# Kernel tuning notes

Measured on AMD Instinct MI355X. Metric: run time of the kernel, lower is better.

The kernel has to match this reference:

```python
import jax, jax.numpy as jnp
import numpy as np

B, T, D, H, QK, V, M = 2, 2048, 1024, 16, 64, 64, 1024
SOFTCAP = 50.0


def apply_rope(x, positions, max_wavelength=10000.0):
    # x: (B, T, H, d), positions: (T,)
    d = x.shape[-1]
    fraction = 2.0 * jnp.arange(d // 2, dtype=jnp.float32) / d
    timescale = max_wavelength ** fraction                      # (d/2,)
    sinusoid = positions.astype(jnp.float32)[:, None] / timescale  # (T, d/2)
    sin = jnp.sin(sinusoid)[:, None, :]  # (T, 1, d/2) broadcasts over heads
    cos = jnp.cos(sinusoid)[:, None, :]
    x1, x2 = jnp.split(x, 2, axis=-1)
    out = jnp.concatenate([x1 * cos - x2 * sin, x2 * cos + x1 * sin], axis=-1)
    return out.astype(x.dtype)


def rms_norm(x, scale, eps=1e-6):
    var = jnp.mean(jnp.square(x.astype(jnp.float32)), axis=-1, keepdims=True)
    normed = x * jax.lax.rsqrt(var + eps).astype(x.dtype)
    return normed * (1.0 + scale).astype(x.dtype)


def setup_inputs() -> dict:
    key = jax.random.key(0)
    ks = jax.random.split(key, 10)
    s = 0.02
    # key-padding mask: per-batch kv valid lengths (all rows have >=1536 valid keys)
    kv_lens = jnp.array([1536, 2048], dtype=jnp.int32)
    mask = (jnp.arange(T)[None, :] < kv_lens[:, None])  # (B, Tk)
    mask = jnp.broadcast_to(mask[:, None, None, :], (B, 1, T, T))
    return {
        "q": jax.random.normal(ks[0], (B, T, D), jnp.float32),
        "kv": jax.random.normal(ks[1], (B, T, D), jnp.float32),
        "mask": mask,
        "q_positions": jnp.arange(T, dtype=jnp.int32),
        "kv_positions": jnp.arange(T, dtype=jnp.int32),
        "wq": jax.random.normal(ks[2], (D, H * QK), jnp.float32) * s,
        "bq": jnp.zeros((H * QK,), jnp.float32),
        "wk": jax.random.normal(ks[3], (D, H * QK), jnp.float32) * s,
        "bk": jnp.zeros((H * QK,), jnp.float32),
        "wv": jax.random.normal(ks[4], (D, H * V), jnp.float32) * s,
        "bv": jnp.zeros((H * V,), jnp.float32),
        "q_scale": jnp.zeros((QK,), jnp.float32),
        "k_scale": jnp.zeros((QK,), jnp.float32),
        "wo": jax.random.normal(ks[5], (H * V, M), jnp.float32) * s,
        "bo": jnp.zeros((M,), jnp.float32),
    }


def reference(q, kv, mask, q_positions, kv_positions,
              wq, bq, wk, bk, wv, bv, q_scale, k_scale, wo, bo):
    qh = (q @ wq + bq).reshape(B, T, H, QK)
    kh = (kv @ wk + bk).reshape(B, T, H, QK)
    vh = (kv @ wv + bv).reshape(B, T, H, V)
    # QK RMSNorm
    qh = rms_norm(qh, q_scale)
    kh = rms_norm(kh, k_scale)
    # RoPE
    qh = apply_rope(qh, q_positions)
    kh = apply_rope(kh, kv_positions)
    # softcapped, masked attention
    logits = jnp.einsum("bthd,bThd->bhtT", qh, kh) / np.sqrt(QK).astype(jnp.float32)
    logits = SOFTCAP * jnp.tanh(logits / SOFTCAP)
    logits = jnp.where(mask, logits, -1e9)
    log_probs = jax.nn.log_softmax(logits, axis=-1)
    probs = jnp.exp(log_probs)
    probs = jnp.where(mask, probs, 0.0)
    # normalized attention entropy (B, H, T)
    entropy = -jnp.sum(probs * log_probs, axis=-1) / jnp.log(mask.sum(axis=-1))
    attn = jnp.einsum("bhtT,bThd->bthd", probs, vh).reshape(B, T, H * V)
    out = attn @ wo + bo
    return out, entropy
```

## Files before the change

### kernel.cpp

```cpp
#include <hip/hip_runtime.h>

#define BB 2
#define TT 2048
#define DD 1024
#define HH 16
#define QKD 64
#define VD 64
#define MD 1024

typedef _Float16 half4 __attribute__((ext_vector_type(4)));
typedef _Float16 half8 __attribute__((ext_vector_type(8)));
typedef __fp16 fp16x2 __attribute__((ext_vector_type(2)));
typedef float f32x4 __attribute__((ext_vector_type(4)));
typedef unsigned short us8 __attribute__((ext_vector_type(8)));
typedef unsigned short us4 __attribute__((ext_vector_type(4)));

__device__ __forceinline__ unsigned short f2h(float x){
    union { _Float16 h; unsigned short u; } c; c.h = (_Float16)x; return c.u;
}

__device__ __forceinline__ void gl16(const void* g, void* l){
    __builtin_amdgcn_global_load_lds(
        (const __attribute__((address_space(1))) void*)g,
        (__attribute__((address_space(3))) void*)l, 16, 0, 0);
}

__global__ __launch_bounds__(256) void k_prep(const float* __restrict__ q,
                                              const float* __restrict__ kv,
                                              unsigned short* __restrict__ q_bf,
                                              unsigned short* __restrict__ kv_bf,
                                              const float* __restrict__ w0,
                                              const float* __restrict__ w1,
                                              const float* __restrict__ w2,
                                              const float* __restrict__ w3,
                                              unsigned short* __restrict__ o0,
                                              unsigned short* __restrict__ o1,
                                              unsigned short* __restrict__ o2,
                                              unsigned short* __restrict__ o3,
                                              const int* __restrict__ qpos,
                                              const int* __restrict__ kpos,
                                              float* __restrict__ tabq,
                                              float* __restrict__ tabk,
                                              const unsigned char* __restrict__ mask,
                                              int* __restrict__ kvlen){
    __shared__ float smem[64*65];
    int bid = blockIdx.x, tid = threadIdx.x;
    if (bid < 8192){
        const int n = BB*TT*DD/4;
        int idx = bid*256 + tid;
        const float* src = (idx < n) ? q : kv;
        unsigned short* dst = (idx < n) ? q_bf : kv_bf;
        int i = ((idx < n) ? idx : idx - n)*4;
        const float4 v = *(const float4*)(src + i);
        us4 o; o.x = f2h(v.x); o.y = f2h(v.y); o.z = f2h(v.z); o.w = f2h(v.w);
        *(us4*)(dst + i) = o;
    } else if (bid < 9216){
        int idx2 = bid - 8192;
        int z = idx2 >> 8;
        int rc2 = idx2 & 255;
        const float* in = (z==0) ? w0 : (z==1) ? w1 : (z==2) ? w2 : w3;
        unsigned short* out = (z==0) ? o0 : (z==1) ? o1 : (z==2) ? o2 : o3;
        float (*ts)[65] = (float(*)[65])smem;
        int r0 = (rc2 & 15)*64, c0 = (rc2 >> 4)*64;
        int lr = tid >> 4, lc = (tid & 15)*4;
#pragma unroll
        for (int i = 0; i < 4; ++i){
            const float4 v = *(const float4*)(in + (long)(r0 + lr + i*16)*1024 + c0 + lc);
            ts[lr+i*16][lc+0] = v.x; ts[lr+i*16][lc+1] = v.y;
            ts[lr+i*16][lc+2] = v.z; ts[lr+i*16][lc+3] = v.w;
        }
        __syncthreads();
        int oc = tid >> 2, rc = (tid & 3)*16;
        int ocp = oc;
        if (z < 2){
            int blk = oc >> 4;
            ocp = (blk == 1) ? oc + 16 : ((blk == 2) ? oc - 16 : oc);
        }
        us8 o0v, o1v;
#pragma unroll
        for (int j = 0; j < 8; ++j){ o0v[j] = f2h(ts[rc+j][ocp]); o1v[j] = f2h(ts[rc+8+j][ocp]); }
        *(us8*)(out + (long)(c0+oc)*1024 + r0 + rc)     = o0v;
        *(us8*)(out + (long)(c0+oc)*1024 + r0 + rc + 8) = o1v;
    } else if (bid < 9728){
        int gi = (bid - 9216)*256 + tid;
        const int* pos = (gi < 65536) ? qpos : kpos;
        float* tab = (gi < 65536) ? tabq : tabk;
        int idx = gi & 65535;
        int t = idx >> 5, f = idx & 31;
        float invts = expf(-((float)f*(1.f/32.f)) * 9.210340371976184f);
        float ph = (float)pos[t]*invts;
        ((float2*)tab)[idx] = make_float2(sinf(ph), cosf(ph));
    } else {
        int* red = (int*)smem;
        int b = bid - 9728;
        bool bytemode = (mask[1] != 0);
        int cnt = 0;
        for (int j = tid; j < TT; j += 256){
            long e = (long)b*TT*TT + j;
            if (bytemode) cnt += (mask[e] != 0);
            else          cnt += (((const unsigned int*)mask)[e] != 0);
        }
        red[tid] = cnt; __syncthreads();
        for (int s = 128; s > 0; s >>= 1){ if (tid < s) red[tid] += red[tid+s]; __syncthreads(); }
        if (tid == 0) kvlen[b] = red[0];
    }
}

#define GEMM_CORE(A_, Bt_, abase, bbase)                                            \
    int srow = l >> 3;                                                              \
    int scol = ((l & 7) ^ srow)*8;                                                  \
    int swb = lg ^ (li & 7);                                                        \
    const unsigned short* ga[4]; const unsigned short* gb[2];                       \
    _Pragma("unroll")                                                               \
    for (int i = 0; i < 4; ++i) ga[i] = A_  + (long)(m0 + w*32 + i*8 + srow)*1024 + scol; \
    _Pragma("unroll")                                                               \
    for (int i = 0; i < 2; ++i) gb[i] = Bt_ + (long)(n0 + w*16 + i*8 + srow)*1024 + scol; \
    _Pragma("unroll")                                                               \
    for (int i = 0; i < 4; ++i) gl16(ga[i], abase + (w*32 + i*8)*128);              \
    _Pragma("unroll")                                                               \
    for (int i = 0; i < 2; ++i) gl16(gb[i], bbase + (w*16 + i*8)*128);              \
    __syncthreads();                                                                \
    for (int ks = 0; ks < 16; ++ks){                                                \
        int cur = ks & 1;                                                           \
        if (ks + 1 < 16){                                                           \
            char* an = abase + (cur^1)*16384;                                       \
            char* bn = bbase + (cur^1)*8192;                                        \
            _Pragma("unroll")                                                       \
            for (int i = 0; i < 4; ++i){ ga[i] += 64; gl16(ga[i], an + (w*32 + i*8)*128); } \
            _Pragma("unroll")                                                       \
            for (int i = 0; i < 2; ++i){ gb[i] += 64; gl16(gb[i], bn + (w*16 + i*8)*128); } \
        }                                                                           \
        const char* ac = abase + cur*16384;                                         \
        const char* bc = bbase + cur*8192;                                          \
        _Pragma("unroll")                                                           \
        for (int kk = 0; kk < 2; ++kk){                                             \
            int co = ((kk*4) ^ swb)*16;                                             \
            half8 af[4], bf[2];                                                     \
            _Pragma("unroll")                                                       \
            for (int mi = 0; mi < 4; ++mi) af[mi] = *(const half8*)(ac + (wm + mi*16 + li)*128 + co); \
            _Pragma("unroll")                                                       \
            for (int ni = 0; ni < 2; ++ni) bf[ni] = *(const half8*)(bc + (wn + ni*16 + li)*128 + co); \
            _Pragma("unroll")                                                       \
            for (int mi = 0; mi < 4; ++mi)                                          \
                _Pragma("unroll")                                                   \
                for (int ni = 0; ni < 2; ++ni)                                      \
                    acc[mi][ni] = __builtin_amdgcn_mfma_f32_16x16x32_f16(af[mi], bf[ni], acc[mi][ni], 0, 0, 0); \
        }                                                                           \
        __syncthreads();                                                            \
    }

__global__ __launch_bounds__(256) void k_gemm3(const unsigned short* __restrict__ q_bf,
                                               const unsigned short* __restrict__ kv_bf,
                                               const unsigned short* __restrict__ wqt,
                                               const unsigned short* __restrict__ wkt,
                                               const unsigned short* __restrict__ wvt,
                                               const float* __restrict__ bq,
                                               const float* __restrict__ bk,
                                               const float* __restrict__ bv,
                                               const float* __restrict__ qscale,
                                               const float* __restrict__ kscale,
                                               const float* __restrict__ tabq,
                                               const float* __restrict__ tabk,
                                               unsigned short* __restrict__ Qr,
                                               unsigned short* __restrict__ Kr,
                                               unsigned short* __restrict__ VTb){
    __shared__ float4 smem_[3072];
    char* abase = (char*)smem_;
    char* bbase = abase + 32768;
    int flat = blockIdx.x;
    int virt = (flat & 7)*192 + (flat >> 3);
    int z = virt >> 9;
    int rem = virt & 511;
    int m0 = (rem >> 4)*128;
    int nx = rem & 15;
    int n0 = nx*64;
    const unsigned short* A  = (z == 0) ? q_bf : kv_bf;
    const unsigned short* Bt = (z == 0) ? wqt : (z == 1) ? wkt : wvt;

    int tid = threadIdx.x, l = tid & 63, w = tid >> 6;
    int lg = l >> 4, li = l & 15;
    int wm = (w >> 1)*64, wn = (w & 1)*32;
    f32x4 zero = {0.f,0.f,0.f,0.f};
    f32x4 acc[4][2];
#pragma unroll
    for (int mi = 0; mi < 4; ++mi){ acc[mi][0] = zero; acc[mi][1] = zero; }
    GEMM_CORE(A, Bt, abase, bbase)

    int hd = nx;
    if (z < 2){
        const float* bias  = (z == 0) ? bq : bk;
        const float* scale = (z == 0) ? qscale : kscale;
        const float* tab   = (z == 0) ? tabq : tabk;
        unsigned short* out = (z == 0) ? Qr : Kr;
        float* hs = (float*)smem_;
        int d0 = (wn >> 1) + li;
        float b0 = bias[hd*64 + d0];
        float b1 = bias[hd*64 + d0 + 32];
        float ssp[4][4];
#pragma unroll
        for (int mi = 0; mi < 4; ++mi)
#pragma unroll
            for (int r = 0; r < 4; ++r){
                float x0 = acc[mi][0][r] + b0;
                float x1 = acc[mi][1][r] + b1;
                ssp[mi][r] = x0*x0 + x1*x1;
            }
#pragma unroll
        for (int m = 1; m < 16; m <<= 1)
#pragma unroll
            for (int mi = 0; mi < 4; ++mi)
#pragma unroll
                for (int r = 0; r < 4; ++r) ssp[mi][r] += __shfl_xor(ssp[mi][r], m);
        if (li == 0){
#pragma unroll
            for (int mi = 0; mi < 4; ++mi)
#pragma unroll
                for (int r = 0; r < 4; ++r)
                    hs[(wm + mi*16 + lg*4 + r)*2 + (w & 1)] = ssp[mi][r];
        }
        __syncthreads();
        float sc0 = 1.f + scale[d0];
        float sc1 = 1.f + scale[d0 + 32];
#pragma unroll
        for (int mi = 0; mi < 4; ++mi)
#pragma unroll
            for (int r = 0; r < 4; ++r){
                int row = wm + mi*16 + lg*4 + r;
                float ss = hs[row*2] + hs[row*2 + 1];
                float rstd = rsqrtf(ss*(1.f/64.f) + 1e-6f);
                float x0 = (acc[mi][0][r] + b0)*rstd*sc0;
                float x1 = (acc[mi][1][r] + b1)*rstd*sc1;
                int gm = m0 + row;
                int bb = gm >> 11, t = gm & 2047;
                float2 scv = ((const float2*)tab)[t*32 + d0];
                float o0 = x0*scv.y - x1*scv.x;
                float o1 = x1*scv.y + x0*scv.x;
                long obase = ((long)(bb*HH + hd)*TT + t)*64;
                out[obase + d0]      = f2h(o0);
                out[obase + d0 + 32] = f2h(o1);
            }
    } else {
        float* Tt = (float*)smem_;
#pragma unroll
        for (int mi = 0; mi < 4; ++mi)
#pragma unroll
            for (int ni = 0; ni < 2; ++ni){
                int col = wn + ni*16 + li;
                float bb = bv[hd*64 + col];
#pragma unroll
                for (int r = 0; r < 4; ++r)
                    Tt[col*133 + wm + mi*16 + lg*4 + r] = acc[mi][ni][r] + bb;
            }
        __syncthreads();
        int bb2 = m0 >> 11, t0 = m0 & 2047;
        int vd = tid >> 2, sg = (tid & 3)*32;
        long ob = ((long)(bb2*HH + hd)*64 + vd)*TT + t0 + sg;
#pragma unroll
        for (int c = 0; c < 4; ++c){
            us8 o;
#pragma unroll
            for (int j = 0; j < 8; ++j) o[j] = f2h(Tt[vd*133 + sg + c*8 + j]);
            *(us8*)(VTb + ob + c*8) = o;
        }
    }
}

__global__ __launch_bounds__(256) void k_gemm(const unsigned short* __restrict__ A,
                                              const unsigned short* __restrict__ Bt,
                                              const float* __restrict__ bias,
                                              float* __restrict__ C, int N){
    __shared__ float4 smem_[3072];
    char* abase = (char*)smem_;
    char* bbase = abase + 32768;
    int flat = blockIdx.x;
    int virt = (flat & 7)*64 + (flat >> 3);
    int m0 = (virt >> 4)*128, n0 = (virt & 15)*64;
    int tid = threadIdx.x, l = tid & 63, w = tid >> 6;
    int lg = l >> 4, li = l & 15;
    int wm = (w >> 1)*64, wn = (w & 1)*32;
    f32x4 zero = {0.f,0.f,0.f,0.f};
    f32x4 acc[4][2];
#pragma unroll
    for (int mi = 0; mi < 4; ++mi){ acc[mi][0] = zero; acc[mi][1] = zero; }
    GEMM_CORE(A, Bt, abase, bbase)
#pragma unroll
    for (int mi = 0; mi < 4; ++mi){
#pragma unroll
        for (int ni = 0; ni < 2; ++ni){
            int row = m0 + wm + mi*16 + lg*4;
            int col = n0 + wn + ni*16 + li;
            float bb = bias[col];
#pragma unroll
            for (int r = 0; r < 4; ++r)
                C[(long)(row + r)*N + col] = acc[mi][ni][r] + bb;
        }
    }
}

__global__ __launch_bounds__(256) void k_attn(const unsigned short* __restrict__ Qr,
                                              const unsigned short* __restrict__ Kr,
                                              const unsigned short* __restrict__ VT,
                                              const int* __restrict__ kvlen,
                                              unsigned short* __restrict__ attnb,
                                              float* __restrict__ ent){
    __shared__ unsigned short Ks[2][64][64];
    __shared__ unsigned short Vs[2][64][64];
    int tid = threadIdx.x;
    int l = tid & 63, w = tid >> 6;
    int lg = l >> 4, li = l & 15;
    int flat = blockIdx.x;
    int xcd = flat & 7;
    int idx = flat >> 3;
    int qt = idx & 31;
    int g = idx >> 5;
    int bh = xcd*2 + (g & 1) + (g >> 1)*16;
    int b = bh >> 4, h = bh & 15;
    long qk0 = (long)bh * TT * 64;
    long vt0 = (long)bh * 64 * TT;
    int kvl = kvlen[b];
    int q0 = qt*64 + w*16;

    half8 qf[2];
#pragma unroll
    for (int kk = 0; kk < 2; ++kk)
        qf[kk] = *(const half8*)(Qr + qk0 + (long)(q0 + li)*64 + kk*32 + lg*8);

    int srow = l >> 3;
    int scol = ((l & 7) ^ srow)*8;
    const unsigned short* gK0 = Kr + qk0 + (long)(w*8 + srow)*64 + scol;
    const unsigned short* gK1 = gK0 + 32*64;
    const unsigned short* gV0 = VT + vt0 + (long)(w*8 + srow)*TT + scol;
    const unsigned short* gV1 = gV0 + (long)32*TT;
    char* ksb = (char*)Ks;
    char* vsb = (char*)Vs;
    int swb = (lg >> 1) ^ (li & 7);
    int off8 = (lg & 1)*8;

    gl16(gK0, ksb + w*8*128);
    gl16(gK1, ksb + (32 + w*8)*128);
    gl16(gV0, vsb + w*8*128);
    gl16(gV1, vsb + (32 + w*8)*128);
    __syncthreads();

    f32x4 zero = {0.f,0.f,0.f,0.f};
    f32x4 oacc[4];
#pragma unroll
    for (int jv = 0; jv < 4; ++jv) oacc[jv] = zero;
    float l4[4]  = {0.f,0.f,0.f,0.f};
    float s14[4] = {0.f,0.f,0.f,0.f};

    const float PA = 0.18033688f;
    const float PB = -3.7570183e-7f;

    int nkv = (kvl + 63) >> 6;
    for (int kt = 0; kt < nkv; ++kt){
        int cur = kt & 1;
        const char* kc = ksb + cur*8192;
        const char* vc = vsb + cur*8192;
        if (kt + 1 < nkv){
            gK0 += 4096; gK1 += 4096;
            gV0 += 64;   gV1 += 64;
            char* kn = ksb + (cur^1)*8192;
            char* vn = vsb + (cur^1)*8192;
            gl16(gK0, kn + w*8*128);
            gl16(gK1, kn + (32 + w*8)*128);
            gl16(gV0, vn + w*8*128);
            gl16(gV1, vn + (32 + w*8)*128);
        }
        f32x4 sacc[4];
#pragma unroll
        for (int jt = 0; jt < 4; ++jt) sacc[jt] = zero;
#pragma unroll
        for (int kk = 0; kk < 2; ++kk){
            int co = ((kk*4 + lg) ^ (li & 7))*16;
#pragma unroll
            for (int jt = 0; jt < 4; ++jt){
                half8 kf = *(const half8*)(kc + (jt*16 + li)*128 + co);
                sacc[jt] = __builtin_amdgcn_mfma_f32_16x16x32_f16(kf, qf[kk], sacc[jt], 0, 0, 0);
            }
        }
        float xs2[4][4];
        bool tail = (kt*64 + 64 > kvl);
        if (tail){
#pragma unroll
            for (int jt = 0; jt < 4; ++jt){
#pragma unroll
                for (int r = 0; r < 4; ++r){
                    float u = sacc[jt][r];
                    float v = u*(PA + u*u*PB);
                    xs2[jt][r] = (kt*64 + jt*16 + lg*4 + r < kvl) ? v : -1e30f;
                }
            }
        } else {
#pragma unroll
            for (int jt = 0; jt < 4; ++jt){
#pragma unroll
                for (int r = 0; r < 4; ++r){
                    float u = sacc[jt][r];
                    xs2[jt][r] = u*(PA + u*u*PB);
                }
            }
        }
        float p[4][4];
#pragma unroll
        for (int jt = 0; jt < 4; ++jt){
#pragma unroll
            for (int r = 0; r < 4; ++r){
                float pp = exp2f(xs2[jt][r]);
                p[jt][r] = pp;
                l4[r]  += pp;
                s14[r] += pp * xs2[jt][r];
            }
        }
        half4 pa[4];
#pragma unroll
        for (int kk = 0; kk < 4; ++kk){
            union { half4 v; fp16x2 h2[2]; } up;
            up.h2[0] = __builtin_amdgcn_cvt_pkrtz(p[kk][0], p[kk][1]);
            up.h2[1] = __builtin_amdgcn_cvt_pkrtz(p[kk][2], p[kk][3]);
            pa[kk] = up.v;
        }
#pragma unroll
        for (int kk = 0; kk < 4; ++kk){
            int co = (((kk*2) ^ swb))*16 + off8;
#pragma unroll
            for (int jv = 0; jv < 4; ++jv){
                half4 vf = *(const half4*)(vc + (jv*16 + li)*128 + co);
                oacc[jv] = __builtin_amdgcn_mfma_f32_16x16x16f16(pa[kk], vf, oacc[jv], 0, 0, 0);
            }
        }
        __syncthreads();
    }

    float l_r  = (l4[0] + l4[1]) + (l4[2] + l4[3]);
    float s1_r = (s14[0] + s14[1]) + (s14[2] + s14[3]);
    l_r  += __shfl_xor(l_r, 16);  l_r  += __shfl_xor(l_r, 32);
    s1_r += __shfl_xor(s1_r, 16); s1_r += __shfl_xor(s1_r, 32);

    float invl = 1.f / l_r;
    float invr[4];
#pragma unroll
    for (int r = 0; r < 4; ++r) invr[r] = __shfl(invl, lg*4 + r);
#pragma unroll
    for (int jv = 0; jv < 4; ++jv){
#pragma unroll
        for (int r = 0; r < 4; ++r){
            int qrow = q0 + lg*4 + r;
            attnb[((long)b*TT + qrow)*1024 + h*64 + jv*16 + li] = f2h(oacc[jv][r]*invr[r]);
        }
    }
    if (l < 16){
        const float LN2 = 0.6931471805599453f;
        float lse = logf(l_r);
        float s1n = s1_r*LN2;
        ent[(long)bh*TT + q0 + li] = (lse - s1n*invl) / logf((float)kvl);
    }
}

extern "C" void kernel_launch(void* const* d_in, const int* in_sizes, int n_in,
                              void* d_out, int out_size, void* d_ws, size_t ws_size,
                              hipStream_t stream){
    (void)in_sizes; (void)n_in; (void)out_size; (void)ws_size;
    const float* q      = (const float*)d_in[0];
    const float* kv     = (const float*)d_in[1];
    const unsigned char* mask = (const unsigned char*)d_in[2];
    const int*   qpos   = (const int*)d_in[3];
    const int*   kpos   = (const int*)d_in[4];
    const float* wq     = (const float*)d_in[5];
    const float* bq     = (const float*)d_in[6];
    const float* wk     = (const float*)d_in[7];
    const float* bk     = (const float*)d_in[8];
    const float* wv     = (const float*)d_in[9];
    const float* bv     = (const float*)d_in[10];
    const float* qscale = (const float*)d_in[11];
    const float* kscale = (const float*)d_in[12];
    const float* wo     = (const float*)d_in[13];
    const float* bo     = (const float*)d_in[14];
    float* out = (float*)d_out;
    float* ent = out + (long)BB*TT*MD;

    char* ws = (char*)d_ws;
    unsigned short* wqt   = (unsigned short*)(ws);
    unsigned short* wkt   = (unsigned short*)(ws + 2097152L);
    unsigned short* wvt   = (unsigned short*)(ws + 4194304L);
    unsigned short* wot   = (unsigned short*)(ws + 6291456L);
    unsigned short* q_bf  = (unsigned short*)(ws + 8388608L);
    unsigned short* kv_bf = (unsigned short*)(ws + 16777216L);
    unsigned short* Qr    = (unsigned short*)(ws + 25165824L);
    unsigned short* Kr    = (unsigned short*)(ws + 33554432L);
    unsigned short* VTb   = (unsigned short*)(ws + 41943040L);
    unsigned short* attnb = (unsigned short*)(ws + 50331648L);
    float*          tabq  = (float*)(ws + 58720256L);
    float*          tabk  = (float*)(ws + 59244544L);
    int*            kvln  = (int*)(ws + 59768832L);

    k_prep<<<9730, 256, 0, stream>>>(q, kv, q_bf, kv_bf,
                                     wq, wk, wv, wo, wqt, wkt, wvt, wot,
                                     qpos, kpos, tabq, tabk, mask, kvln);

    k_gemm3<<<1536, 256, 0, stream>>>(q_bf, kv_bf, wqt, wkt, wvt,
                                      bq, bk, bv, qscale, kscale,
                                      tabq, tabk, Qr, Kr, VTb);

    k_attn<<<1024, 256, 0, stream>>>(Qr, Kr, VTb, kvln, attnb, ent);

    k_gemm<<<512, 256, 0, stream>>>(attnb, wot, bo, out, 1024);
}
```

Before: 143.8 us.

## Load K and V fragments directly from global memory in attention kernel

Removes the double-buffered LDS staging of K and V tiles (global_load_lds plus barriers) and has each wave read its MFMA fragments straight from global memory through the cache. This drops the per-iteration __syncthreads and the shared-memory footprint, which may raise occupancy. In exchange, each of the four waves in a block redundantly fetches the same K/V tiles, and the loads are exposed in the loop without explicit prefetch, relying on L1/L2 hits and the compiler to hide latency.

```diff
diff --git a/kernel.cpp b/kernel.cpp
--- a/kernel.cpp
+++ b/kernel.cpp
@@ -303,8 +303,6 @@
                                               const int* __restrict__ kvlen,
                                               unsigned short* __restrict__ attnb,
                                               float* __restrict__ ent){
-    __shared__ unsigned short Ks[2][64][64];
-    __shared__ unsigned short Vs[2][64][64];
     int tid = threadIdx.x;
     int l = tid & 63, w = tid >> 6;
     int lg = l >> 4, li = l & 15;
@@ -325,23 +323,6 @@
     for (int kk = 0; kk < 2; ++kk)
         qf[kk] = *(const half8*)(Qr + qk0 + (long)(q0 + li)*64 + kk*32 + lg*8);
 
-    int srow = l >> 3;
-    int scol = ((l & 7) ^ srow)*8;
-    const unsigned short* gK0 = Kr + qk0 + (long)(w*8 + srow)*64 + scol;
-    const unsigned short* gK1 = gK0 + 32*64;
-    const unsigned short* gV0 = VT + vt0 + (long)(w*8 + srow)*TT + scol;
-    const unsigned short* gV1 = gV0 + (long)32*TT;
-    char* ksb = (char*)Ks;
-    char* vsb = (char*)Vs;
-    int swb = (lg >> 1) ^ (li & 7);
-    int off8 = (lg & 1)*8;
-
-    gl16(gK0, ksb + w*8*128);
-    gl16(gK1, ksb + (32 + w*8)*128);
-    gl16(gV0, vsb + w*8*128);
-    gl16(gV1, vsb + (32 + w*8)*128);
-    __syncthreads();
-
     f32x4 zero = {0.f,0.f,0.f,0.f};
     f32x4 oacc[4];
 #pragma unroll
@@ -352,30 +333,19 @@
     const float PA = 0.18033688f;
     const float PB = -3.7570183e-7f;
 
+    const unsigned short* Kp = Kr + qk0 + (long)li*64 + lg*8;
+    const unsigned short* Vp = VT + vt0 + (long)li*TT + lg*4;
+
     int nkv = (kvl + 63) >> 6;
     for (int kt = 0; kt < nkv; ++kt){
-        int cur = kt & 1;
-        const char* kc = ksb + cur*8192;
-        const char* vc = vsb + cur*8192;
-        if (kt + 1 < nkv){
-            gK0 += 4096; gK1 += 4096;
-            gV0 += 64;   gV1 += 64;
-            char* kn = ksb + (cur^1)*8192;
-            char* vn = vsb + (cur^1)*8192;
-            gl16(gK0, kn + w*8*128);
-            gl16(gK1, kn + (32 + w*8)*128);
-            gl16(gV0, vn + w*8*128);
-            gl16(gV1, vn + (32 + w*8)*128);
-        }
         f32x4 sacc[4];
 #pragma unroll
         for (int jt = 0; jt < 4; ++jt) sacc[jt] = zero;
 #pragma unroll
         for (int kk = 0; kk < 2; ++kk){
-            int co = ((kk*4 + lg) ^ (li & 7))*16;
 #pragma unroll
             for (int jt = 0; jt < 4; ++jt){
-                half8 kf = *(const half8*)(kc + (jt*16 + li)*128 + co);
+                half8 kf = *(const half8*)(Kp + (long)(kt*64 + jt*16)*64 + kk*32);
                 sacc[jt] = __builtin_amdgcn_mfma_f32_16x16x32_f16(kf, qf[kk], sacc[jt], 0, 0, 0);
             }
         }
@@ -422,14 +392,12 @@
         }
 #pragma unroll
         for (int kk = 0; kk < 4; ++kk){
-            int co = (((kk*2) ^ swb))*16 + off8;
 #pragma unroll
             for (int jv = 0; jv < 4; ++jv){
-                half4 vf = *(const half4*)(vc + (jv*16 + li)*128 + co);
+                half4 vf = *(const half4*)(Vp + (long)(jv*16)*TT + kt*64 + kk*16);
                 oacc[jv] = __builtin_amdgcn_mfma_f32_16x16x16f16(pa[kk], vf, oacc[jv], 0, 0, 0);
             }
         }
-        __syncthreads();
     }
 
     float l_r  = (l4[0] + l4[1]) + (l4[2] + l4[3]);
```

Measured after the change: 360.3 us. 151% more time.
